# Optimization experiments

Hardware: AMD Instinct MI355X
Metric: run time of the kernel (lower is better)

The kernel has to match this reference:

```python
import jax, jax.numpy as jnp
import numpy as np

N_NODES = 50000
N_EDGES = 150000
EMB = 64
IN_DIM = 32
LN_EPS = 1e-5


def setup_inputs() -> dict:
    key = jax.random.key(0)
    k1, k2, k3, k4 = jax.random.split(key, 4)
    h = jax.random.normal(k1, (N_NODES, EMB), dtype=jnp.float32)
    edge_attr = jax.random.normal(k2, (N_EDGES, IN_DIM), dtype=jnp.float32)
    edge_index = jax.random.randint(k3, (2, N_EDGES), 0, N_NODES, dtype=jnp.int64)
    # xavier_uniform for [EMB*EMB, IN_DIM] weight
    limit = float(np.sqrt(6.0 / (EMB * EMB + IN_DIM)))
    W = jax.random.uniform(k4, (EMB * EMB, IN_DIM), dtype=jnp.float32,
                           minval=-limit, maxval=limit)
    b = jnp.zeros((EMB * EMB,), dtype=jnp.float32)
    gamma = jnp.ones((EMB,), dtype=jnp.float32)
    beta = jnp.zeros((EMB,), dtype=jnp.float32)
    return {"h": h, "edge_attr": edge_attr, "W": W, "b": b,
            "gamma": gamma, "beta": beta, "edge_index": edge_index}


def reference(h, edge_attr, W, b, gamma, beta, edge_index):
    M = edge_attr.shape[0]
    E = h.shape[1]
    # per-edge transform matrix from edge features: [M, E, E]
    m = (edge_attr @ W.T + b).reshape(M, E, E)
    # gather target-node features and apply per-edge matvec: [M, E]
    h_j = h[edge_index[1]]
    msg = jnp.einsum('mef,mf->me', m, h_j)
    # scatter-add messages to source nodes
    aggr = jax.ops.segment_sum(msg, edge_index[0], num_segments=h.shape[0])
    # residual + LayerNorm
    x = h + aggr
    mu = jnp.mean(x, axis=-1, keepdims=True)
    var = jnp.mean(jnp.square(x - mu), axis=-1, keepdims=True)
    y = (x - mu) * jax.lax.rsqrt(var + LN_EPS)
    return y * gamma + beta
```

## Files before the change

### kernel.cpp

```cpp
#include <hip/hip_runtime.h>
#include <math.h>

#define N_NODES 50000
#define N_EDGES 150000
#define LN_EPS 1e-5f

#define BM 256
#define WM 64

typedef _Float16 f16x8 __attribute__((ext_vector_type(8)));
typedef _Float16 f16x4 __attribute__((ext_vector_type(4)));
typedef _Float16 f16x2 __attribute__((ext_vector_type(2)));
typedef float    f32x4 __attribute__((ext_vector_type(4)));

static __device__ __forceinline__ f16x2 pkrtz(float a, float b) {
    auto p = __builtin_amdgcn_cvt_pkrtz(a, b);
    f16x2 r; r[0] = (_Float16)p[0]; r[1] = (_Float16)p[1];
    return r;
}

__global__ void prep_kernel(const float* __restrict__ W, const float* __restrict__ b,
                            f16x8* __restrict__ WtF) {
    int tid = blockIdx.x * 256 + threadIdx.x;
    if (tid >= 66 * 4 * 64) return;
    int l  = tid & 63;
    int nb = (tid >> 6) & 3;
    int c  = tid >> 8;
    int k0 = (l >> 4) << 3;
    int e  = nb * 16 + (l & 15);
    const float* src = (c < 64) ? &W[(e * 64 + c) * 32 + k0]
                                : &b[e * 64 + (c - 64) * 32 + k0];
    float4 v0 = *(const float4*)src;
    float4 v1 = *(const float4*)(src + 4);
    f16x8 o;
    o[0] = (_Float16)v0.x; o[1] = (_Float16)v0.y; o[2] = (_Float16)v0.z; o[3] = (_Float16)v0.w;
    o[4] = (_Float16)v1.x; o[5] = (_Float16)v1.y; o[6] = (_Float16)v1.z; o[7] = (_Float16)v1.w;
    WtF[tid] = o;
}

__global__ void init_kernel(const float* __restrict__ h, float* __restrict__ out) {
    int tid = blockIdx.x * 256 + threadIdx.x;
    ((float4*)out)[tid] = ((const float4*)h)[tid];
}

__launch_bounds__(256, 3)
__global__ void edge_kernel(const float* __restrict__ ea,
                            const float* __restrict__ h,
                            const int*   __restrict__ ei,
                            const f16x8* __restrict__ WtF,
                            float* __restrict__ out)
{
    __shared__ _Float16 s_hj[BM][68];
    __shared__ int      s_src[BM];

    const int t = threadIdx.x;
    const int m_base = blockIdx.x * BM;

    {
        int gm = m_base + t;
        if (gm < N_EDGES) {
            s_src[t] = ei[gm];
            const float4* hr = (const float4*)&h[(size_t)ei[N_EDGES + gm] * 64];
            #pragma unroll
            for (int j = 0; j < 16; ++j) {
                float4 v = hr[j];
                f16x2 p0 = pkrtz(v.x, v.y);
                f16x2 p1 = pkrtz(v.z, v.w);
                f16x4 o; o[0] = p0[0]; o[1] = p0[1]; o[2] = p1[0]; o[3] = p1[1];
                *(f16x4*)&s_hj[t][j * 4] = o;
            }
        } else {
            s_src[t] = -1;
            f16x4 z = (f16x4){0, 0, 0, 0};
            #pragma unroll
            for (int j = 0; j < 16; ++j)
                *(f16x4*)&s_hj[t][j * 4] = z;
        }
    }

    const int lane = t & 63;
    const int w    = t >> 6;
    const int r16  = lane & 15;
    const int g    = lane >> 4;
    const int k0   = g * 8;
    const int row0 = w * WM;
    int rows[4];
    #pragma unroll
    for (int a = 0; a < 4; ++a) rows[a] = row0 + a * 16 + r16;

    f16x2 eap[4][4];
    #pragma unroll
    for (int a = 0; a < 4; ++a) {
        int gm = m_base + rows[a];
        if (gm < N_EDGES) {
            float4 v0 = *(const float4*)&ea[(size_t)gm * 32 + k0];
            float4 v1 = *(const float4*)&ea[(size_t)gm * 32 + k0 + 4];
            eap[a][0] = pkrtz(v0.x, v0.y);
            eap[a][1] = pkrtz(v0.z, v0.w);
            eap[a][2] = pkrtz(v1.x, v1.y);
            eap[a][3] = pkrtz(v1.z, v1.w);
        } else {
            #pragma unroll
            for (int i = 0; i < 4; ++i) eap[a][i] = (f16x2){0, 0};
        }
    }

    f32x4 acc[4][4];
    #pragma unroll
    for (int a = 0; a < 4; ++a)
        #pragma unroll
        for (int nb = 0; nb < 4; ++nb)
            acc[a][nb] = (f32x4){0.f, 0.f, 0.f, 0.f};

    __syncthreads();

    f16x8 b0[4], b1[4], b2[4];
    #pragma unroll
    for (int nb = 0; nb < 4; ++nb) b0[nb] = WtF[(0 * 4 + nb) * 64 + lane];
    #pragma unroll
    for (int nb = 0; nb < 4; ++nb) b1[nb] = WtF[(1 * 4 + nb) * 64 + lane];
    #pragma unroll
    for (int nb = 0; nb < 4; ++nb) b2[nb] = WtF[(2 * 4 + nb) * 64 + lane];

    _Float16 hc[4];
    #pragma unroll
    for (int a = 0; a < 4; ++a) hc[a] = s_hj[rows[a]][0];

    auto step = [&](int c, f16x8* bb, bool loadnext) {
        _Float16 hn[4] = {0, 0, 0, 0};
        if (loadnext) {
            #pragma unroll
            for (int a = 0; a < 4; ++a) hn[a] = s_hj[rows[a]][c + 1];
        }
        #pragma unroll
        for (int a = 0; a < 4; ++a) {
            f16x2 hs; hs[0] = hc[a]; hs[1] = hc[a];
            f16x2 p0 = eap[a][0] * hs;
            f16x2 p1 = eap[a][1] * hs;
            f16x2 p2 = eap[a][2] * hs;
            f16x2 p3 = eap[a][3] * hs;
            f16x8 va;
            va[0] = p0[0]; va[1] = p0[1]; va[2] = p1[0]; va[3] = p1[1];
            va[4] = p2[0]; va[5] = p2[1]; va[6] = p3[0]; va[7] = p3[1];
            #pragma unroll
            for (int nb = 0; nb < 4; ++nb)
                acc[a][nb] = __builtin_amdgcn_mfma_f32_16x16x32_f16(va, bb[nb], acc[a][nb], 0, 0, 0);
        }
        #pragma unroll
        for (int a = 0; a < 4; ++a) hc[a] = hn[a];
    };

    for (int c = 0; c < 63; c += 3) {
        step(c, b0, true);
        #pragma unroll
        for (int nb = 0; nb < 4; ++nb) b0[nb] = WtF[((c + 3) * 4 + nb) * 64 + lane];
        step(c + 1, b1, true);
        #pragma unroll
        for (int nb = 0; nb < 4; ++nb) b1[nb] = WtF[((c + 4) * 4 + nb) * 64 + lane];
        step(c + 2, b2, true);
        #pragma unroll
        for (int nb = 0; nb < 4; ++nb) b2[nb] = WtF[((c + 5) * 4 + nb) * 64 + lane];
    }
    step(63, b0, false);

    #pragma unroll
    for (int half = 0; half < 2; ++half) {
        f16x8* bb = half ? b2 : b1;
        #pragma unroll
        for (int a = 0; a < 4; ++a) {
            f16x4 lo = *(const f16x4*)&s_hj[rows[a]][half * 32 + k0];
            f16x4 hi = *(const f16x4*)&s_hj[rows[a]][half * 32 + k0 + 4];
            f16x8 va;
            va[0] = lo[0]; va[1] = lo[1]; va[2] = lo[2]; va[3] = lo[3];
            va[4] = hi[0]; va[5] = hi[1]; va[6] = hi[2]; va[7] = hi[3];
            #pragma unroll
            for (int nb = 0; nb < 4; ++nb)
                acc[a][nb] = __builtin_amdgcn_mfma_f32_16x16x32_f16(va, bb[nb], acc[a][nb], 0, 0, 0);
        }
    }

    #pragma unroll
    for (int a = 0; a < 4; ++a) {
        #pragma unroll
        for (int r = 0; r < 4; ++r) {
            int srcn = s_src[row0 + a * 16 + g * 4 + r];
            if (srcn >= 0) {
                #pragma unroll
                for (int nb = 0; nb < 4; ++nb)
                    atomicAdd(&out[(size_t)srcn * 64 + nb * 16 + r16], acc[a][nb][r]);
            }
        }
    }
}

__global__ void ln_kernel(const float* __restrict__ gamma, const float* __restrict__ beta,
                          float* __restrict__ out) {
    int row = blockIdx.x * 4 + (threadIdx.x >> 6);
    int lane = threadIdx.x & 63;
    if (row >= N_NODES) return;
    float x = out[row * 64 + lane];
    float s = x;
    #pragma unroll
    for (int o = 32; o; o >>= 1) s += __shfl_xor(s, o);
    float mu = s * (1.0f / 64.0f);
    float d = x - mu;
    float v = d * d;
    #pragma unroll
    for (int o = 32; o; o >>= 1) v += __shfl_xor(v, o);
    float var = v * (1.0f / 64.0f);
    float r = rsqrtf(var + LN_EPS);
    out[row * 64 + lane] = d * r * gamma[lane] + beta[lane];
}

extern "C" void kernel_launch(void* const* d_in, const int* in_sizes, int n_in,
                              void* d_out, int out_size, void* d_ws, size_t ws_size,
                              hipStream_t stream) {
    const float* h     = (const float*)d_in[0];
    const float* ea    = (const float*)d_in[1];
    const float* W     = (const float*)d_in[2];
    const float* b     = (const float*)d_in[3];
    const float* gamma = (const float*)d_in[4];
    const float* beta  = (const float*)d_in[5];
    const int*   ei    = (const int*)d_in[6];
    float* out = (float*)d_out;

    f16x8* WtF = (f16x8*)d_ws;

    prep_kernel<<<66, 256, 0, stream>>>(W, b, WtF);
    init_kernel<<<(N_NODES * 64 / 4 + 255) / 256, 256, 0, stream>>>(h, out);
    edge_kernel<<<(N_EDGES + BM - 1) / BM, 256, 0, stream>>>(ea, h, ei, WtF, out);
    ln_kernel<<<(N_NODES + 3) / 4, 256, 0, stream>>>(gamma, beta, out);
}
```

Baseline: 158.1 us.

## Split edge kernel reduction over c into two blocks and merge setup launches

```diff
diff --git a/kernel.cpp b/kernel.cpp
--- a/kernel.cpp
+++ b/kernel.cpp
@@ -19,28 +19,29 @@
     return r;
 }
 
-__global__ void prep_kernel(const float* __restrict__ W, const float* __restrict__ b,
-                            f16x8* __restrict__ WtF) {
-    int tid = blockIdx.x * 256 + threadIdx.x;
-    if (tid >= 66 * 4 * 64) return;
-    int l  = tid & 63;
-    int nb = (tid >> 6) & 3;
-    int c  = tid >> 8;
-    int k0 = (l >> 4) << 3;
-    int e  = nb * 16 + (l & 15);
-    const float* src = (c < 64) ? &W[(e * 64 + c) * 32 + k0]
-                                : &b[e * 64 + (c - 64) * 32 + k0];
-    float4 v0 = *(const float4*)src;
-    float4 v1 = *(const float4*)(src + 4);
-    f16x8 o;
-    o[0] = (_Float16)v0.x; o[1] = (_Float16)v0.y; o[2] = (_Float16)v0.z; o[3] = (_Float16)v0.w;
-    o[4] = (_Float16)v1.x; o[5] = (_Float16)v1.y; o[6] = (_Float16)v1.z; o[7] = (_Float16)v1.w;
-    WtF[tid] = o;
-}
-
-__global__ void init_kernel(const float* __restrict__ h, float* __restrict__ out) {
-    int tid = blockIdx.x * 256 + threadIdx.x;
-    ((float4*)out)[tid] = ((const float4*)h)[tid];
+__global__ void setup_kernel(const float* __restrict__ W, const float* __restrict__ b,
+                             const float* __restrict__ h,
+                             f16x8* __restrict__ WtF, float* __restrict__ out) {
+    int bid = blockIdx.x;
+    if (bid < 66) {
+        int tid = bid * 256 + threadIdx.x;
+        int l  = tid & 63;
+        int nb = (tid >> 6) & 3;
+        int c  = tid >> 8;
+        int k0 = (l >> 4) << 3;
+        int e  = nb * 16 + (l & 15);
+        const float* src = (c < 64) ? &W[(e * 64 + c) * 32 + k0]
+                                    : &b[e * 64 + (c - 64) * 32 + k0];
+        float4 v0 = *(const float4*)src;
+        float4 v1 = *(const float4*)(src + 4);
+        f16x8 o;
+        o[0] = (_Float16)v0.x; o[1] = (_Float16)v0.y; o[2] = (_Float16)v0.z; o[3] = (_Float16)v0.w;
+        o[4] = (_Float16)v1.x; o[5] = (_Float16)v1.y; o[6] = (_Float16)v1.z; o[7] = (_Float16)v1.w;
+        WtF[tid] = o;
+    } else {
+        int tid = (bid - 66) * 256 + threadIdx.x;
+        ((float4*)out)[tid] = ((const float4*)h)[tid];
+    }
 }
 
 __launch_bounds__(256, 3)
@@ -53,8 +54,11 @@
     __shared__ _Float16 s_hj[BM][68];
     __shared__ int      s_src[BM];
 
-    const int t = threadIdx.x;
-    const int m_base = blockIdx.x * BM;
+    const int t     = threadIdx.x;
+    const int tile  = blockIdx.x >> 1;
+    const int s     = blockIdx.x & 1;
+    const int m_base = tile * BM;
+    const int cbase  = s * 32;
 
     {
         int gm = m_base + t;
@@ -116,15 +120,15 @@
 
     f16x8 b0[4], b1[4], b2[4];
     #pragma unroll
-    for (int nb = 0; nb < 4; ++nb) b0[nb] = WtF[(0 * 4 + nb) * 64 + lane];
-    #pragma unroll
-    for (int nb = 0; nb < 4; ++nb) b1[nb] = WtF[(1 * 4 + nb) * 64 + lane];
-    #pragma unroll
-    for (int nb = 0; nb < 4; ++nb) b2[nb] = WtF[(2 * 4 + nb) * 64 + lane];
+    for (int nb = 0; nb < 4; ++nb) b0[nb] = WtF[((cbase + 0) * 4 + nb) * 64 + lane];
+    #pragma unroll
+    for (int nb = 0; nb < 4; ++nb) b1[nb] = WtF[((cbase + 1) * 4 + nb) * 64 + lane];
+    #pragma unroll
+    for (int nb = 0; nb < 4; ++nb) b2[nb] = WtF[((cbase + 2) * 4 + nb) * 64 + lane];
 
     _Float16 hc[4];
     #pragma unroll
-    for (int a = 0; a < 4; ++a) hc[a] = s_hj[rows[a]][0];
+    for (int a = 0; a < 4; ++a) hc[a] = s_hj[rows[a]][cbase];
 
     auto step = [&](int c, f16x8* bb, bool loadnext) {
         _Float16 hn[4] = {0, 0, 0, 0};
@@ -150,7 +154,7 @@
         for (int a = 0; a < 4; ++a) hc[a] = hn[a];
     };
 
-    for (int c = 0; c < 63; c += 3) {
+    for (int c = cbase; c < cbase + 30; c += 3) {
         step(c, b0, true);
         #pragma unroll
         for (int nb = 0; nb < 4; ++nb) b0[nb] = WtF[((c + 3) * 4 + nb) * 64 + lane];
@@ -161,21 +165,28 @@
         #pragma unroll
         for (int nb = 0; nb < 4; ++nb) b2[nb] = WtF[((c + 5) * 4 + nb) * 64 + lane];
     }
-    step(63, b0, false);
-
-    #pragma unroll
-    for (int half = 0; half < 2; ++half) {
-        f16x8* bb = half ? b2 : b1;
-        #pragma unroll
-        for (int a = 0; a < 4; ++a) {
-            f16x4 lo = *(const f16x4*)&s_hj[rows[a]][half * 32 + k0];
-            f16x4 hi = *(const f16x4*)&s_hj[rows[a]][half * 32 + k0 + 4];
-            f16x8 va;
-            va[0] = lo[0]; va[1] = lo[1]; va[2] = lo[2]; va[3] = lo[3];
-            va[4] = hi[0]; va[5] = hi[1]; va[6] = hi[2]; va[7] = hi[3];
-            #pragma unroll
-            for (int nb = 0; nb < 4; ++nb)
-                acc[a][nb] = __builtin_amdgcn_mfma_f32_16x16x32_f16(va, bb[nb], acc[a][nb], 0, 0, 0);
+    step(cbase + 30, b0, true);
+    if (s) {
+        #pragma unroll
+        for (int nb = 0; nb < 4; ++nb) b0[nb] = WtF[(65 * 4 + nb) * 64 + lane];
+    }
+    step(cbase + 31, b1, false);
+
+    if (s) {
+        #pragma unroll
+        for (int half = 0; half < 2; ++half) {
+            f16x8* bb = half ? b0 : b2;
+            #pragma unroll
+            for (int a = 0; a < 4; ++a) {
+                f16x4 lo = *(const f16x4*)&s_hj[rows[a]][half * 32 + k0];
+                f16x4 hi = *(const f16x4*)&s_hj[rows[a]][half * 32 + k0 + 4];
+                f16x8 va;
+                va[0] = lo[0]; va[1] = lo[1]; va[2] = lo[2]; va[3] = lo[3];
+                va[4] = hi[0]; va[5] = hi[1]; va[6] = hi[2]; va[7] = hi[3];
+                #pragma unroll
+                for (int nb = 0; nb < 4; ++nb)
+                    acc[a][nb] = __builtin_amdgcn_mfma_f32_16x16x32_f16(va, bb[nb], acc[a][nb], 0, 0, 0);
+            }
         }
     }
 
@@ -226,8 +237,7 @@
 
     f16x8* WtF = (f16x8*)d_ws;
 
-    prep_kernel<<<66, 256, 0, stream>>>(W, b, WtF);
-    init_kernel<<<(N_NODES * 64 / 4 + 255) / 256, 256, 0, stream>>>(h, out);
-    edge_kernel<<<(N_EDGES + BM - 1) / BM, 256, 0, stream>>>(ea, h, ei, WtF, out);
+    setup_kernel<<<66 + 3125, 256, 0, stream>>>(W, b, h, WtF, out);
+    edge_kernel<<<2 * ((N_EDGES + BM - 1) / BM), 256, 0, stream>>>(ea, h, ei, WtF, out);
     ln_kernel<<<(N_NODES + 3) / 4, 256, 0, stream>>>(gamma, beta, out);
 }
```

After: 200.0 us. +26.5%, slower.

## Split edge tile N dimension across two waves and merge setup kernels

Applied to the files above, without the earlier changes.

```diff
diff --git a/kernel.cpp b/kernel.cpp
--- a/kernel.cpp
+++ b/kernel.cpp
@@ -19,31 +19,32 @@
     return r;
 }
 
-__global__ void prep_kernel(const float* __restrict__ W, const float* __restrict__ b,
-                            f16x8* __restrict__ WtF) {
-    int tid = blockIdx.x * 256 + threadIdx.x;
-    if (tid >= 66 * 4 * 64) return;
-    int l  = tid & 63;
-    int nb = (tid >> 6) & 3;
-    int c  = tid >> 8;
-    int k0 = (l >> 4) << 3;
-    int e  = nb * 16 + (l & 15);
-    const float* src = (c < 64) ? &W[(e * 64 + c) * 32 + k0]
-                                : &b[e * 64 + (c - 64) * 32 + k0];
-    float4 v0 = *(const float4*)src;
-    float4 v1 = *(const float4*)(src + 4);
-    f16x8 o;
-    o[0] = (_Float16)v0.x; o[1] = (_Float16)v0.y; o[2] = (_Float16)v0.z; o[3] = (_Float16)v0.w;
-    o[4] = (_Float16)v1.x; o[5] = (_Float16)v1.y; o[6] = (_Float16)v1.z; o[7] = (_Float16)v1.w;
-    WtF[tid] = o;
-}
-
-__global__ void init_kernel(const float* __restrict__ h, float* __restrict__ out) {
-    int tid = blockIdx.x * 256 + threadIdx.x;
-    ((float4*)out)[tid] = ((const float4*)h)[tid];
-}
-
-__launch_bounds__(256, 3)
+__global__ void setup_kernel(const float* __restrict__ W, const float* __restrict__ b,
+                             const float* __restrict__ h,
+                             f16x8* __restrict__ WtF, float* __restrict__ out) {
+    int bid = blockIdx.x;
+    if (bid < 66) {
+        int tid = bid * 256 + threadIdx.x;
+        int l  = tid & 63;
+        int nb = (tid >> 6) & 3;
+        int c  = tid >> 8;
+        int k0 = (l >> 4) << 3;
+        int e  = nb * 16 + (l & 15);
+        const float* src = (c < 64) ? &W[(e * 64 + c) * 32 + k0]
+                                    : &b[e * 64 + (c - 64) * 32 + k0];
+        float4 v0 = *(const float4*)src;
+        float4 v1 = *(const float4*)(src + 4);
+        f16x8 o;
+        o[0] = (_Float16)v0.x; o[1] = (_Float16)v0.y; o[2] = (_Float16)v0.z; o[3] = (_Float16)v0.w;
+        o[4] = (_Float16)v1.x; o[5] = (_Float16)v1.y; o[6] = (_Float16)v1.z; o[7] = (_Float16)v1.w;
+        WtF[tid] = o;
+    } else {
+        int tid = (bid - 66) * 256 + threadIdx.x;
+        ((float4*)out)[tid] = ((const float4*)h)[tid];
+    }
+}
+
+__launch_bounds__(512, 4)
 __global__ void edge_kernel(const float* __restrict__ ea,
                             const float* __restrict__ h,
                             const int*   __restrict__ ei,
@@ -57,33 +58,38 @@
     const int m_base = blockIdx.x * BM;
 
     {
-        int gm = m_base + t;
+        int row  = t >> 1;
+        int half = t & 1;
+        int gm   = m_base + row;
         if (gm < N_EDGES) {
-            s_src[t] = ei[gm];
-            const float4* hr = (const float4*)&h[(size_t)ei[N_EDGES + gm] * 64];
-            #pragma unroll
-            for (int j = 0; j < 16; ++j) {
+            if (half == 0) s_src[row] = ei[gm];
+            const float4* hr = (const float4*)&h[(size_t)ei[N_EDGES + gm] * 64 + half * 32];
+            #pragma unroll
+            for (int j = 0; j < 8; ++j) {
                 float4 v = hr[j];
                 f16x2 p0 = pkrtz(v.x, v.y);
                 f16x2 p1 = pkrtz(v.z, v.w);
                 f16x4 o; o[0] = p0[0]; o[1] = p0[1]; o[2] = p1[0]; o[3] = p1[1];
-                *(f16x4*)&s_hj[t][j * 4] = o;
+                *(f16x4*)&s_hj[row][half * 32 + j * 4] = o;
             }
         } else {
-            s_src[t] = -1;
+            if (half == 0) s_src[row] = -1;
             f16x4 z = (f16x4){0, 0, 0, 0};
             #pragma unroll
-            for (int j = 0; j < 16; ++j)
-                *(f16x4*)&s_hj[t][j * 4] = z;
+            for (int j = 0; j < 8; ++j)
+                *(f16x4*)&s_hj[row][half * 32 + j * 4] = z;
         }
     }
 
     const int lane = t & 63;
-    const int w    = t >> 6;
+    const int wid  = t >> 6;
+    const int wrow = wid & 3;
+    const int wn   = wid >> 2;
+    const int nb0  = wn * 2;
     const int r16  = lane & 15;
     const int g    = lane >> 4;
     const int k0   = g * 8;
-    const int row0 = w * WM;
+    const int row0 = wrow * WM;
     int rows[4];
     #pragma unroll
     for (int a = 0; a < 4; ++a) rows[a] = row0 + a * 16 + r16;
@@ -105,22 +111,22 @@
         }
     }
 
-    f32x4 acc[4][4];
+    f32x4 acc[4][2];
     #pragma unroll
     for (int a = 0; a < 4; ++a)
         #pragma unroll
-        for (int nb = 0; nb < 4; ++nb)
+        for (int nb = 0; nb < 2; ++nb)
             acc[a][nb] = (f32x4){0.f, 0.f, 0.f, 0.f};
 
     __syncthreads();
 
-    f16x8 b0[4], b1[4], b2[4];
-    #pragma unroll
-    for (int nb = 0; nb < 4; ++nb) b0[nb] = WtF[(0 * 4 + nb) * 64 + lane];
-    #pragma unroll
-    for (int nb = 0; nb < 4; ++nb) b1[nb] = WtF[(1 * 4 + nb) * 64 + lane];
-    #pragma unroll
-    for (int nb = 0; nb < 4; ++nb) b2[nb] = WtF[(2 * 4 + nb) * 64 + lane];
+    f16x8 b0[2], b1[2], b2[2];
+    #pragma unroll
+    for (int j = 0; j < 2; ++j) b0[j] = WtF[(0 * 4 + nb0 + j) * 64 + lane];
+    #pragma unroll
+    for (int j = 0; j < 2; ++j) b1[j] = WtF[(1 * 4 + nb0 + j) * 64 + lane];
+    #pragma unroll
+    for (int j = 0; j < 2; ++j) b2[j] = WtF[(2 * 4 + nb0 + j) * 64 + lane];
 
     _Float16 hc[4];
     #pragma unroll
@@ -143,8 +149,8 @@
             va[0] = p0[0]; va[1] = p0[1]; va[2] = p1[0]; va[3] = p1[1];
             va[4] = p2[0]; va[5] = p2[1]; va[6] = p3[0]; va[7] = p3[1];
             #pragma unroll
-            for (int nb = 0; nb < 4; ++nb)
-                acc[a][nb] = __builtin_amdgcn_mfma_f32_16x16x32_f16(va, bb[nb], acc[a][nb], 0, 0, 0);
+            for (int j = 0; j < 2; ++j)
+                acc[a][j] = __builtin_amdgcn_mfma_f32_16x16x32_f16(va, bb[j], acc[a][j], 0, 0, 0);
         }
         #pragma unroll
         for (int a = 0; a < 4; ++a) hc[a] = hn[a];
@@ -153,13 +159,13 @@
     for (int c = 0; c < 63; c += 3) {
         step(c, b0, true);
         #pragma unroll
-        for (int nb = 0; nb < 4; ++nb) b0[nb] = WtF[((c + 3) * 4 + nb) * 64 + lane];
+        for (int j = 0; j < 2; ++j) b0[j] = WtF[((c + 3) * 4 + nb0 + j) * 64 + lane];
         step(c + 1, b1, true);
         #pragma unroll
-        for (int nb = 0; nb < 4; ++nb) b1[nb] = WtF[((c + 4) * 4 + nb) * 64 + lane];
+        for (int j = 0; j < 2; ++j) b1[j] = WtF[((c + 4) * 4 + nb0 + j) * 64 + lane];
         step(c + 2, b2, true);
         #pragma unroll
-        for (int nb = 0; nb < 4; ++nb) b2[nb] = WtF[((c + 5) * 4 + nb) * 64 + lane];
+        for (int j = 0; j < 2; ++j) b2[j] = WtF[((c + 5) * 4 + nb0 + j) * 64 + lane];
     }
     step(63, b0, false);
 
@@ -174,8 +180,8 @@
             va[0] = lo[0]; va[1] = lo[1]; va[2] = lo[2]; va[3] = lo[3];
             va[4] = hi[0]; va[5] = hi[1]; va[6] = hi[2]; va[7] = hi[3];
             #pragma unroll
-            for (int nb = 0; nb < 4; ++nb)
-                acc[a][nb] = __builtin_amdgcn_mfma_f32_16x16x32_f16(va, bb[nb], acc[a][nb], 0, 0, 0);
+            for (int j = 0; j < 2; ++j)
+                acc[a][j] = __builtin_amdgcn_mfma_f32_16x16x32_f16(va, bb[j], acc[a][j], 0, 0, 0);
         }
     }
 
@@ -186,8 +192,8 @@
             int srcn = s_src[row0 + a * 16 + g * 4 + r];
             if (srcn >= 0) {
                 #pragma unroll
-                for (int nb = 0; nb < 4; ++nb)
-                    atomicAdd(&out[(size_t)srcn * 64 + nb * 16 + r16], acc[a][nb][r]);
+                for (int j = 0; j < 2; ++j)
+                    atomicAdd(&out[(size_t)srcn * 64 + (nb0 + j) * 16 + r16], acc[a][j][r]);
             }
         }
     }
@@ -226,8 +232,7 @@
 
     f16x8* WtF = (f16x8*)d_ws;
 
-    prep_kernel<<<66, 256, 0, stream>>>(W, b, WtF);
-    init_kernel<<<(N_NODES * 64 / 4 + 255) / 256, 256, 0, stream>>>(h, out);
-    edge_kernel<<<(N_EDGES + BM - 1) / BM, 256, 0, stream>>>(ea, h, ei, WtF, out);
+    setup_kernel<<<66 + 3125, 256, 0, stream>>>(W, b, h, WtF, out);
+    edge_kernel<<<(N_EDGES + BM - 1) / BM, 512, 0, stream>>>(ea, h, ei, WtF, out);
     ln_kernel<<<(N_NODES + 3) / 4, 256, 0, stream>>>(gamma, beta, out);
 }
```

After: 163.0 us. +3.1%, slower.
